# Performance work log

Measured on AMD Instinct MI355X. Metric: run time of the kernel, lower is better.

The kernel has to match this reference:

```python
import jax, jax.numpy as jnp
import numpy as np

H = 8
SPLIT = 1
# deterministic stand-in for random.shuffle(range(8)) in the original
_PERM = np.random.RandomState(0).permutation(H)
SERIES_IDX = jnp.asarray(_PERM[SPLIT:])  # 7 heads
CROSS_IDX = jnp.asarray(_PERM[:SPLIT])   # 1 head


def setup_inputs() -> dict:
    key = jax.random.key(0)
    ks = jax.random.split(key, 5)
    B, L, E = 8, 1024, 64
    shp = (B, L, H, E)
    return {
        "queries": jax.random.normal(ks[0], shp, dtype=jnp.float32),
        "keys": jax.random.normal(ks[1], shp, dtype=jnp.float32),
        "keysT": jax.random.normal(ks[2], shp, dtype=jnp.float32),
        "values": jax.random.normal(ks[3], shp, dtype=jnp.float32),
        "valuesT": jax.random.normal(ks[4], shp, dtype=jnp.float32),
    }


def reference(queries, keys, keysT, values, valuesT):
    B, L, _, E = queries.shape
    scale = 1.0 / jnp.sqrt(jnp.asarray(E, dtype=queries.dtype))
    neg_inf = jnp.asarray(-jnp.inf, dtype=queries.dtype)

    # head split (gather along head dim)
    sq = queries[:, :, SERIES_IDX]   # [B,L,7,E]
    sk = keys[:, :, SERIES_IDX]      # [B,S,7,E]
    sv = values[:, :, SERIES_IDX]    # [B,S,7,D]
    cq = queries[:, :, CROSS_IDX]    # [B,L,1,E]
    ckT = keysT[:, :, CROSS_IDX]     # [B,C,1,E]
    cvT = valuesT[:, :, CROSS_IDX]   # [B,C,1,D]

    # causal mask: True above the diagonal -> disallowed
    causal = jnp.triu(jnp.ones((L, L), dtype=bool), k=1)  # [L,L]

    # series branch
    scores = jnp.einsum('blne,bsne->bnls', sq, sk)  # [B,7,L,S]
    scores = jnp.where(causal[None, None], neg_inf, scores * scale)
    series = jax.nn.softmax(scores, axis=-1)
    V = jnp.einsum('bhls,bshd->blhd', series, sv)   # [B,L,7,D]

    # cross branch
    cscores = jnp.einsum('blme,bcme->bmlc', cq, ckT)  # [B,1,L,C]
    cscores = jnp.where(causal[None, None], neg_inf, cscores * scale)
    crosses = jax.nn.softmax(cscores, axis=-1)
    V_cross = jnp.einsum('bhlc,bchd->blhd', crosses, cvT)  # [B,L,1,D]

    return jnp.concatenate([V, V_cross], axis=2)  # [B,L,8,D]
```

## Files before the change

kernel.cpp:

```cpp
#include <hip/hip_runtime.h>
#include <math.h>

#define Lq 1024
#define Hq 8
#define Eq 64
#define LDW 72

#define SRC_HEAD_PACKED 0x64503712u

typedef __bf16 bf16_t;
typedef __bf16 bf16x8 __attribute__((ext_vector_type(8)));
typedef short  shortx4 __attribute__((ext_vector_type(4)));
typedef float  floatx4 __attribute__((ext_vector_type(4)));

__device__ __forceinline__ bf16x8 cvt8(const float4 a, const float4 b) {
    bf16x8 r;
    r[0] = (bf16_t)a.x; r[1] = (bf16_t)a.y; r[2] = (bf16_t)a.z; r[3] = (bf16_t)a.w;
    r[4] = (bf16_t)b.x; r[5] = (bf16_t)b.y; r[6] = (bf16_t)b.z; r[7] = (bf16_t)b.w;
    return r;
}

__global__ __launch_bounds__(256, 2)
void attn_mfma(const float* __restrict__ Q, const float* __restrict__ Ks,
               const float* __restrict__ KTs, const float* __restrict__ Vs,
               const float* __restrict__ VTs, float* __restrict__ out) {
    const int p    = blockIdx.x;
    const int slot = blockIdx.y;
    const int b    = blockIdx.z;
    const int h    = (SRC_HEAD_PACKED >> (slot * 4)) & 0xF;
    const float* __restrict__ Kp = (slot == 7) ? KTs : Ks;
    const float* __restrict__ Vp = (slot == 7) ? VTs : Vs;
    const int pA = p, pB = 15 - p;

    const int tid  = threadIdx.x;
    const int wv   = tid >> 6;
    const int lane = tid & 63;
    const int ln16 = lane & 15;
    const int quad = lane >> 4;

    __shared__ alignas(16) unsigned short k_lds[2][64][LDW];
    __shared__ alignas(16) unsigned short vt_lds[2][64][LDW];

    const float qs = 0.125f * 1.44269504f;
    bf16x8 qfA[2], qfB[2];
    {
        const int rA = pA * 64 + wv * 16 + ln16;
        const int rB = pB * 64 + wv * 16 + ln16;
        const float* qa = Q + (((size_t)b * Lq + rA) * Hq + h) * Eq + quad * 8;
        const float* qb = Q + (((size_t)b * Lq + rB) * Hq + h) * Eq + quad * 8;
        #pragma unroll
        for (int ec = 0; ec < 2; ++ec) {
            float4 f0 = ((const float4*)(qa + ec * 32))[0];
            float4 f1 = ((const float4*)(qa + ec * 32))[1];
            float4 g0 = ((const float4*)(qb + ec * 32))[0];
            float4 g1 = ((const float4*)(qb + ec * 32))[1];
            f0.x*=qs; f0.y*=qs; f0.z*=qs; f0.w*=qs; f1.x*=qs; f1.y*=qs; f1.z*=qs; f1.w*=qs;
            g0.x*=qs; g0.y*=qs; g0.z*=qs; g0.w*=qs; g1.x*=qs; g1.y*=qs; g1.z*=qs; g1.w*=qs;
            qfA[ec] = cvt8(f0, f1);
            qfB[ec] = cvt8(g0, g1);
        }
    }

    floatx4 OA[4], OB[4];
    #pragma unroll
    for (int i = 0; i < 4; ++i) { OA[i] = (floatx4){0,0,0,0}; OB[i] = (floatx4){0,0,0,0}; }
    float mA = -INFINITY, lA = 0.f, mB = -INFINITY, lB = 0.f;

    const int kj = tid >> 2;
    const int kc = ((((tid & 3) + kj) & 3)) * 16;
    const int vd = lane;
    const int vk = (((tid >> 6) + (vd >> 4)) & 3) * 16;

    float4 kq[4];
    float  vq[16];
    auto load_tile = [&](int kt) {
        const float* kb = Kp + (((size_t)b * Lq + kt * 64 + kj) * Hq + h) * Eq + kc;
        kq[0] = ((const float4*)kb)[0]; kq[1] = ((const float4*)kb)[1];
        kq[2] = ((const float4*)kb)[2]; kq[3] = ((const float4*)kb)[3];
        const float* vb = Vp + (((size_t)b * Lq + kt * 64 + vk) * Hq + h) * Eq + vd;
        #pragma unroll
        for (int i = 0; i < 16; ++i) vq[i] = vb[(size_t)i * (Hq * Eq)];
    };
    auto stage = [&](int buf) {
        *(bf16x8*)&k_lds[buf][kj][kc]     = cvt8(kq[0], kq[1]);
        *(bf16x8*)&k_lds[buf][kj][kc + 8] = cvt8(kq[2], kq[3]);
        const float4* vq4 = (const float4*)vq;
        *(bf16x8*)&vt_lds[buf][vd][vk]     = cvt8(vq4[0], vq4[1]);
        *(bf16x8*)&vt_lds[buf][vd][vk + 8] = cvt8(vq4[2], vq4[3]);
    };

    auto process = [&](const bf16x8 (&qf)[2], bf16x8 (&kf)[4][2], shortx4 (&vf)[4][4],
                       floatx4 (&O)[4], float& m, float& l, bool diag) {
        floatx4 s[4];
        #pragma unroll
        for (int nc = 0; nc < 4; ++nc) {
            floatx4 acc = (floatx4){0,0,0,0};
            acc = __builtin_amdgcn_mfma_f32_16x16x32_bf16(kf[nc][0], qf[0], acc, 0, 0, 0);
            acc = __builtin_amdgcn_mfma_f32_16x16x32_bf16(kf[nc][1], qf[1], acc, 0, 0, 0);
            s[nc] = acc;
        }
        if (diag) {
            const int rin = wv * 16 + ln16;
            #pragma unroll
            for (int nc = 0; nc < 4; ++nc)
                #pragma unroll
                for (int r = 0; r < 4; ++r)
                    if (nc * 16 + quad * 4 + r > rin) s[nc][r] = -INFINITY;
        }
        float mn = s[0][0];
        #pragma unroll
        for (int nc = 0; nc < 4; ++nc)
            #pragma unroll
            for (int r = 0; r < 4; ++r) mn = fmaxf(mn, s[nc][r]);
        mn = fmaxf(mn, __shfl_xor(mn, 16, 64));
        mn = fmaxf(mn, __shfl_xor(mn, 32, 64));
        mn = fmaxf(mn, m);
        const float alpha = __builtin_amdgcn_exp2f(m - mn);
        m = mn;
        float ps = 0.f;
        float pv[4][4];
        #pragma unroll
        for (int nc = 0; nc < 4; ++nc)
            #pragma unroll
            for (int r = 0; r < 4; ++r) { pv[nc][r] = __builtin_amdgcn_exp2f(s[nc][r] - mn); ps += pv[nc][r]; }
        ps += __shfl_xor(ps, 16, 64);
        ps += __shfl_xor(ps, 32, 64);
        l = l * alpha + ps;
        float aO[4];
        #pragma unroll
        for (int r = 0; r < 4; ++r) aO[r] = __shfl(alpha, quad * 4 + r, 64);
        #pragma unroll
        for (int dc = 0; dc < 4; ++dc)
            #pragma unroll
            for (int r = 0; r < 4; ++r) O[dc][r] *= aO[r];
        shortx4 pa[4];
        #pragma unroll
        for (int nc = 0; nc < 4; ++nc) {
            union { shortx4 s4; bf16_t bf[4]; } u;
            u.bf[0] = (bf16_t)pv[nc][0]; u.bf[1] = (bf16_t)pv[nc][1];
            u.bf[2] = (bf16_t)pv[nc][2]; u.bf[3] = (bf16_t)pv[nc][3];
            pa[nc] = u.s4;
        }
        #pragma unroll
        for (int dc = 0; dc < 4; ++dc)
            #pragma unroll
            for (int nc = 0; nc < 4; ++nc)
                O[dc] = __builtin_amdgcn_mfma_f32_16x16x16bf16_1k(pa[nc], vf[dc][nc], O[dc], 0, 0, 0);
    };

    load_tile(0);
    stage(0);
    if (pB >= 1) load_tile(1);
    __syncthreads();

    for (int kt = 0; kt <= pB; ++kt) {
        const int cur = kt & 1, nxt = cur ^ 1;
        if (kt + 1 <= pB) stage(nxt);
        if (kt + 2 <= pB) load_tile(kt + 2);
        bf16x8 kf[4][2];
        shortx4 vf[4][4];
        #pragma unroll
        for (int c = 0; c < 4; ++c) {
            kf[c][0] = *(const bf16x8*)&k_lds[cur][c * 16 + ln16][quad * 8];
            kf[c][1] = *(const bf16x8*)&k_lds[cur][c * 16 + ln16][32 + quad * 8];
        }
        #pragma unroll
        for (int dc = 0; dc < 4; ++dc)
            #pragma unroll
            for (int nc = 0; nc < 4; ++nc)
                vf[dc][nc] = *(const shortx4*)&vt_lds[cur][dc * 16 + ln16][nc * 16 + quad * 4];
        if (kt <= pA) process(qfA, kf, vf, OA, mA, lA, kt == pA);
        process(qfB, kf, vf, OB, mB, lB, kt == pB);
        if (kt < pB) __syncthreads();
    }

    {
        float lo[4];
        #pragma unroll
        for (int r = 0; r < 4; ++r) lo[r] = __shfl(lA, quad * 4 + r, 64);
        const int rowb = pA * 64 + wv * 16 + quad * 4;
        #pragma unroll
        for (int r = 0; r < 4; ++r) {
            const float inv = 1.0f / lo[r];
            float* op = out + (((size_t)b * Lq + rowb + r) * Hq + slot) * Eq + ln16;
            #pragma unroll
            for (int dc = 0; dc < 4; ++dc) op[dc * 16] = OA[dc][r] * inv;
        }
    }
    {
        float lo[4];
        #pragma unroll
        for (int r = 0; r < 4; ++r) lo[r] = __shfl(lB, quad * 4 + r, 64);
        const int rowb = pB * 64 + wv * 16 + quad * 4;
        #pragma unroll
        for (int r = 0; r < 4; ++r) {
            const float inv = 1.0f / lo[r];
            float* op = out + (((size_t)b * Lq + rowb + r) * Hq + slot) * Eq + ln16;
            #pragma unroll
            for (int dc = 0; dc < 4; ++dc) op[dc * 16] = OB[dc][r] * inv;
        }
    }
}

extern "C" void kernel_launch(void* const* d_in, const int* in_sizes, int n_in,
                              void* d_out, int out_size, void* d_ws, size_t ws_size,
                              hipStream_t stream) {
    const float* queries = (const float*)d_in[0];
    const float* keys    = (const float*)d_in[1];
    const float* keysT   = (const float*)d_in[2];
    const float* values  = (const float*)d_in[3];
    const float* valuesT = (const float*)d_in[4];
    float* out = (float*)d_out;

    dim3 grid(8, Hq, 8);
    dim3 block(256);
    attn_mfma<<<grid, block, 0, stream>>>(queries, keys, keysT, values, valuesT, out);
}
```

Measured before the change: 147.1 us.

## Split KV loop across two blocks and merge partial softmax results via workspace

Doubles the grid so each query-tile pair is handled by two blocks that process alternating KV tiles. Each block writes unnormalized partial outputs plus running max and sum to workspace, and an atomic counter lets the last-arriving block merge both halves and write the final output. This targets low occupancy and CU underuse from only 512 blocks. It adds a memset, global partial traffic, and a merge step.

After: 563.9 us. 3.83x slower.

```diff
diff --git a/kernel.cpp b/kernel.cpp
--- a/kernel.cpp
+++ b/kernel.cpp
@@ -7,6 +7,10 @@
 #define LDW 72
 
 #define SRC_HEAD_PACKED 0x64503712u
+
+#define WS_CNT_INTS   4096
+#define PROW          68
+#define PARTIAL_FLTS  (64 * PROW)
 
 typedef __bf16 bf16_t;
 typedef __bf16 bf16x8 __attribute__((ext_vector_type(8)));
@@ -20,11 +24,13 @@
     return r;
 }
 
-__global__ __launch_bounds__(256, 2)
-void attn_mfma(const float* __restrict__ Q, const float* __restrict__ Ks,
-               const float* __restrict__ KTs, const float* __restrict__ Vs,
-               const float* __restrict__ VTs, float* __restrict__ out) {
-    const int p    = blockIdx.x;
+__global__ __launch_bounds__(256, 4)
+void attn_split(const float* __restrict__ Q, const float* __restrict__ Ks,
+                const float* __restrict__ KTs, const float* __restrict__ Vs,
+                const float* __restrict__ VTs, float* __restrict__ out,
+                float* __restrict__ ws) {
+    const int p    = blockIdx.x & 7;
+    const int half = blockIdx.x >> 3;
     const int slot = blockIdx.y;
     const int b    = blockIdx.z;
     const int h    = (SRC_HEAD_PACKED >> (slot * 4)) & 0xF;
@@ -40,6 +46,7 @@
 
     __shared__ alignas(16) unsigned short k_lds[2][64][LDW];
     __shared__ alignas(16) unsigned short vt_lds[2][64][LDW];
+    __shared__ int s_old;
 
     const float qs = 0.125f * 1.44269504f;
     bf16x8 qfA[2], qfB[2];
@@ -148,15 +155,17 @@
                 O[dc] = __builtin_amdgcn_mfma_f32_16x16x16bf16_1k(pa[nc], vf[dc][nc], O[dc], 0, 0, 0);
     };
 
-    load_tile(0);
-    stage(0);
-    if (pB >= 1) load_tile(1);
+    if (half <= pB) {
+        load_tile(half);
+        stage(0);
+        if (half + 2 <= pB) load_tile(half + 2);
+    }
     __syncthreads();
-
-    for (int kt = 0; kt <= pB; ++kt) {
-        const int cur = kt & 1, nxt = cur ^ 1;
-        if (kt + 1 <= pB) stage(nxt);
-        if (kt + 2 <= pB) load_tile(kt + 2);
+    int it = 0;
+    for (int kt = half; kt <= pB; kt += 2, ++it) {
+        const int cur = it & 1, nxt = cur ^ 1;
+        if (kt + 2 <= pB) stage(nxt);
+        if (kt + 4 <= pB) load_tile(kt + 4);
         bf16x8 kf[4][2];
         shortx4 vf[4][4];
         #pragma unroll
@@ -171,35 +180,60 @@
                 vf[dc][nc] = *(const shortx4*)&vt_lds[cur][dc * 16 + ln16][nc * 16 + quad * 4];
         if (kt <= pA) process(qfA, kf, vf, OA, mA, lA, kt == pA);
         process(qfB, kf, vf, OB, mB, lB, kt == pB);
-        if (kt < pB) __syncthreads();
-    }
-
+        if (kt + 2 <= pB) __syncthreads();
+    }
+
+    float* pbase = ws + WS_CNT_INTS;
+    const int idxA = (((b * 8 + slot) * 16 + pA) * 2 + half);
+    const int idxB = (((b * 8 + slot) * 16 + pB) * 2 + half);
     {
-        float lo[4];
-        #pragma unroll
-        for (int r = 0; r < 4; ++r) lo[r] = __shfl(lA, quad * 4 + r, 64);
-        const int rowb = pA * 64 + wv * 16 + quad * 4;
+        float* pb = pbase + (size_t)idxA * PARTIAL_FLTS;
+        #pragma unroll
+        for (int dc = 0; dc < 4; ++dc)
+            #pragma unroll
+            for (int r = 0; r < 4; ++r)
+                pb[(wv * 16 + quad * 4 + r) * PROW + dc * 16 + ln16] = OA[dc][r];
+        if (quad == 0) { pb[(wv * 16 + ln16) * PROW + 64] = mA; pb[(wv * 16 + ln16) * PROW + 65] = lA; }
+    }
+    {
+        float* pb = pbase + (size_t)idxB * PARTIAL_FLTS;
+        #pragma unroll
+        for (int dc = 0; dc < 4; ++dc)
+            #pragma unroll
+            for (int r = 0; r < 4; ++r)
+                pb[(wv * 16 + quad * 4 + r) * PROW + dc * 16 + ln16] = OB[dc][r];
+        if (quad == 0) { pb[(wv * 16 + ln16) * PROW + 64] = mB; pb[(wv * 16 + ln16) * PROW + 65] = lB; }
+    }
+
+    __threadfence();
+    __syncthreads();
+    if (tid == 0) s_old = atomicAdd((int*)ws + ((b * 8 + slot) * 8 + p), 1);
+    __syncthreads();
+    if (s_old == 0) return;
+    __threadfence();
+
+    auto merge_store = [&](floatx4 (&O)[4], float m, float l, int qt, int sidx) {
+        const float* pb = pbase + (size_t)sidx * PARTIAL_FLTS;
         #pragma unroll
         for (int r = 0; r < 4; ++r) {
-            const float inv = 1.0f / lo[r];
-            float* op = out + (((size_t)b * Lq + rowb + r) * Hq + slot) * Eq + ln16;
-            #pragma unroll
-            for (int dc = 0; dc < 4; ++dc) op[dc * 16] = OA[dc][r] * inv;
-        }
-    }
-    {
-        float lo[4];
-        #pragma unroll
-        for (int r = 0; r < 4; ++r) lo[r] = __shfl(lB, quad * 4 + r, 64);
-        const int rowb = pB * 64 + wv * 16 + quad * 4;
-        #pragma unroll
-        for (int r = 0; r < 4; ++r) {
-            const float inv = 1.0f / lo[r];
-            float* op = out + (((size_t)b * Lq + rowb + r) * Hq + slot) * Eq + ln16;
-            #pragma unroll
-            for (int dc = 0; dc < 4; ++dc) op[dc * 16] = OB[dc][r] * inv;
-        }
-    }
+            const int rin = wv * 16 + quad * 4 + r;
+            const float m0 = __shfl(m, quad * 4 + r, 64);
+            const float l0 = __shfl(l, quad * 4 + r, 64);
+            const float m1 = pb[rin * PROW + 64];
+            const float l1 = pb[rin * PROW + 65];
+            const float mm = fmaxf(m0, m1);
+            const float w0 = __builtin_amdgcn_exp2f(m0 - mm);
+            const float w1 = __builtin_amdgcn_exp2f(m1 - mm);
+            const float inv = 1.0f / (l0 * w0 + l1 * w1);
+            float* op = out + (((size_t)b * Lq + qt * 64 + rin) * Hq + slot) * Eq + ln16;
+            #pragma unroll
+            for (int dc = 0; dc < 4; ++dc)
+                op[dc * 16] = (O[dc][r] * w0 + pb[rin * PROW + dc * 16 + ln16] * w1) * inv;
+        }
+    };
+    const int sh = half ^ 1;
+    merge_store(OA, mA, lA, pA, (((b * 8 + slot) * 16 + pA) * 2 + sh));
+    merge_store(OB, mB, lB, pB, (((b * 8 + slot) * 16 + pB) * 2 + sh));
 }
 
 extern "C" void kernel_launch(void* const* d_in, const int* in_sizes, int n_in,
@@ -212,7 +246,10 @@
     const float* valuesT = (const float*)d_in[4];
     float* out = (float*)d_out;
 
-    dim3 grid(8, Hq, 8);
+    hipMemsetAsync(d_ws, 0, WS_CNT_INTS * sizeof(int), stream);
+
+    dim3 grid(16, Hq, 8);
     dim3 block(256);
-    attn_mfma<<<grid, block, 0, stream>>>(queries, keys, keysT, values, valuesT, out);
+    attn_split<<<grid, block, 0, stream>>>(queries, keys, keysT, values, valuesT, out,
+                                           (float*)d_ws);
 }
```
